# Optimization experiments

Measured on AMD Instinct MI355X. Metric: run time of the kernel, lower is better.

The kernel has to match this reference:

```python
import jax, jax.numpy as jnp
import numpy as np

N, F_IN, F_OUT = 8192, 256, 256
NEG_BIG = jnp.float32(-9e15)


def setup_inputs() -> dict:
    key = jax.random.key(0)
    k1, k2, k3, k4 = jax.random.split(key, 4)
    h = jax.random.normal(k1, (N, F_IN), dtype=jnp.float32)
    adj = jax.random.randint(k2, (N, N), 0, 2, dtype=jnp.int32)
    # nn.Linear(in, out): weight [out, in], bias [out]
    lim = 1.0 / np.sqrt(F_IN)
    W = jax.random.uniform(k3, (F_OUT, F_IN), dtype=jnp.float32, minval=-lim, maxval=lim)
    b = jax.random.uniform(k4, (F_OUT,), dtype=jnp.float32, minval=-lim, maxval=lim)
    return {"h": h, "adj": adj, "W": W, "b": b}


def reference(h, adj, W, b):
    n = h.shape[0]
    scale = 1.0 / jnp.sqrt(jnp.asarray(h.shape[1], h.dtype))
    # attention = h @ h.T / sqrt(d)   -> [N, N]
    att = jnp.matmul(h, h.T) * scale
    # masked softmax over rows
    A = jax.nn.softmax(jnp.where(adj > 0, att, NEG_BIG), axis=1)
    eye = jnp.eye(n, dtype=A.dtype)
    A = (A + eye) * 0.5
    # first `k` rows overwritten with identity, k = count of nonzeros in adj[:, 0]
    k = jnp.sum(adj[:, 0] != 0)
    row_is_identity = jnp.arange(n)[:, None] < k  # [N, 1] broadcast mask
    A = jnp.where(row_is_identity, eye, A)
    h_new = jnp.matmul(h, W.T) + b
    return jax.nn.relu(jnp.matmul(A, h_new))
```

## Files before the change

### kernel.cpp

```cpp
#include <hip/hip_runtime.h>


typedef __attribute__((ext_vector_type(8))) short short8;
typedef __attribute__((ext_vector_type(4))) float f32x4;

#define NN 8192
#define DD 256
#define NEGB -1.2983e16f

__device__ __forceinline__ unsigned short f2bf(float f) {
  unsigned u = __builtin_bit_cast(unsigned, f);
  u += 0x7FFFu + ((u >> 16) & 1u);
  return (unsigned short)(u >> 16);
}
__device__ __forceinline__ float bf2f(unsigned short s) {
  unsigned u = ((unsigned)s) << 16;
  return __builtin_bit_cast(float, u);
}
__device__ __forceinline__ f32x4 mfma16(short8 a, short8 b, f32x4 c) {
  return __builtin_amdgcn_mfma_f32_16x16x32_bf16(a, b, c, 0, 0, 0);
}
__device__ __forceinline__ void gld16(const unsigned short* g, unsigned short* l) {
  __builtin_amdgcn_global_load_lds(
      (const __attribute__((address_space(1))) void*)g,
      (__attribute__((address_space(3))) void*)l, 16, 0, 0);
}

__global__ __launch_bounds__(256) void count_k(const int* __restrict__ adj,
                                               int* __restrict__ kout) {
  __shared__ int red[256];
  int gid = blockIdx.x * 256 + threadIdx.x;
  red[threadIdx.x] = (adj[(size_t)gid * NN] != 0);
  __syncthreads();
  for (int off = 128; off; off >>= 1) {
    if (threadIdx.x < off) red[threadIdx.x] += red[threadIdx.x + off];
    __syncthreads();
  }
  if (threadIdx.x == 0) atomicAdd(kout, red[0]);
}

__global__ __launch_bounds__(256) void conv_h(const float* __restrict__ h,
                                              unsigned short* __restrict__ hQf) {
  int gid = blockIdx.x * 256 + threadIdx.x;
  int i = gid >> 6, k4 = (gid & 63) * 4;
  float4 v = *(const float4*)(h + (size_t)i * DD + k4);
  size_t off = ((size_t)((i >> 4) * 8 + (k4 >> 5)) * 64 +
                (((k4 >> 3) & 3) * 16 + (i & 15))) * 8 + (k4 & 7);
  ushort4 o;
  o.x = f2bf(v.x); o.y = f2bf(v.y); o.z = f2bf(v.z); o.w = f2bf(v.w);
  *(ushort4*)(hQf + off) = o;
}

__global__ __launch_bounds__(256) void pack_wf(const float* __restrict__ W,
                                               unsigned short* __restrict__ Wf) {
  int gid = blockIdx.x * 256 + threadIdx.x;
  int l = gid & 63, f = gid >> 6, n16 = f >> 3, kk = f & 7;
  int lr = l & 15, lg = l >> 4;
  const float* src = W + (size_t)(n16 * 16 + lr) * DD + kk * 32 + lg * 8;
  float4 w0 = *(const float4*)src, w1 = *(const float4*)(src + 4);
  short8 o;
  o[0] = (short)f2bf(w0.x); o[1] = (short)f2bf(w0.y);
  o[2] = (short)f2bf(w0.z); o[3] = (short)f2bf(w0.w);
  o[4] = (short)f2bf(w1.x); o[5] = (short)f2bf(w1.y);
  o[6] = (short)f2bf(w1.z); o[7] = (short)f2bf(w1.w);
  *(short8*)(Wf + (size_t)gid * 8) = o;
}

__global__ __launch_bounds__(256) void hnew_k(const unsigned short* __restrict__ hQf,
                                              const unsigned short* __restrict__ Wf,
                                              const float* __restrict__ bias,
                                              unsigned short* __restrict__ hnb,
                                              unsigned short* __restrict__ hnV) {
  const int tid = threadIdx.x, w = tid >> 6, l = tid & 63, lr = l & 15, lg = l >> 4;
  const int row0 = blockIdx.x * 64 + w * 16;

  short8 a[8];
#pragma unroll
  for (int kk = 0; kk < 8; ++kk)
    a[kk] = *(const short8*)(hQf + ((size_t)((row0 >> 4) * 8 + kk) * 64 + l) * 8);

  f32x4 acc[16];
#pragma unroll
  for (int nt = 0; nt < 16; ++nt) acc[nt] = (f32x4){0.f, 0.f, 0.f, 0.f};

#pragma unroll
  for (int kk = 0; kk < 8; ++kk)
#pragma unroll
    for (int nt = 0; nt < 16; ++nt) {
      short8 bf = *(const short8*)(Wf + ((size_t)(nt * 8 + kk) * 64 + l) * 8);
      acc[nt] = mfma16(a[kk], bf, acc[nt]);
    }
#pragma unroll
  for (int nt = 0; nt < 16; ++nt) {
    const int col = nt * 16 + lr;
    const float bv = bias[col];
#pragma unroll
    for (int q = 0; q < 4; ++q) {
      const int row = row0 + lg * 4 + q;
      unsigned short r16 = f2bf(acc[nt][q] + bv);
      hnb[(size_t)row * DD + col] = r16;
      hnV[((size_t)((row >> 5) * 16 + nt) * 64 + ((row >> 3) & 3) * 16 + lr) * 8 +
          (row & 7)] = r16;
    }
  }
}

__global__ __launch_bounds__(256, 2) void attn_k(
    const unsigned short* __restrict__ hQf, const unsigned short* __restrict__ hnV,
    const int* __restrict__ adj, const int* __restrict__ kptr,
    float* __restrict__ pl, unsigned short* __restrict__ pO, int T) {
  __shared__ __align__(16) unsigned short sK[2][8192];
  __shared__ __align__(16) unsigned short sV[2][8192];
  __shared__ __align__(16) unsigned short sP[4][16][40];

  const int tid = threadIdx.x, w = tid >> 6, l = tid & 63, lr = l & 15, lg = l >> 4;
  const int c = blockIdx.x, ty = blockIdx.y;
  const int i0 = ty * 64;
  const int kid = *kptr;
  if (i0 + 64 <= kid) return;

  const int r0 = i0 + w * 16;

  short8 qf[8];
#pragma unroll
  for (int kk = 0; kk < 8; ++kk)
    qf[kk] = *(const short8*)(hQf + ((size_t)((r0 >> 4) * 8 + kk) * 64 + l) * 8);

  f32x4 Oacc[16];
#pragma unroll
  for (int nt = 0; nt < 16; ++nt) Oacc[nt] = (f32x4){0.f, 0.f, 0.f, 0.f};
  float lsum[4] = {0.f, 0.f, 0.f, 0.f};
  const float c1 = 0.09016844005556021f;

  int arow[4];
#pragma unroll
  for (int q = 0; q < 4; ++q) arow[q] = (r0 + lg * 4 + q) * NN;

  const int jt0 = c * T;

  {
    const unsigned short* srcK = hQf + (size_t)jt0 * 8192;
    const unsigned short* srcV = hnV + (size_t)jt0 * 8192;
#pragma unroll
    for (int s = 0; s < 4; ++s) {
      const int so = (w * 4 + s) * 512;
      gld16(srcK + so + l * 8, &sK[0][so]);
      gld16(srcV + so + l * 8, &sV[0][so]);
    }
  }
  int avA[8], avB[8];
#pragma unroll
  for (int nt = 0; nt < 2; ++nt)
#pragma unroll
    for (int q = 0; q < 4; ++q)
      avA[nt * 4 + q] = adj[(size_t)arow[q] + jt0 * 32 + nt * 16 + lr];
  __syncthreads();

#define ATTN_ITER(T_IDX, CUR, MC, MN)                                          \
  {                                                                            \
    const int t_ = (T_IDX);                                                    \
    if (t_ + 1 < T) {    \
      const int jn = jt0 + t_ + 1;                                             \
      const unsigned short* srcK = hQf + (size_t)jn * 8192;                    \
      const unsigned short* srcV = hnV + (size_t)jn * 8192;                    \
      _Pragma("unroll") for (int s = 0; s < 4; ++s) {                          \
        const int so = (w * 4 + s) * 512;                                      \
        gld16(srcK + so + l * 8, &sK[(CUR) ^ 1][so]);                          \
        gld16(srcV + so + l * 8, &sV[(CUR) ^ 1][so]);                          \
      }                                                                        \
      _Pragma("unroll") for (int nt = 0; nt < 2; ++nt)                         \
        _Pragma("unroll") for (int q = 0; q < 4; ++q)                          \
          MN[nt * 4 + q] = adj[(size_t)arow[q] + jn * 32 + nt * 16 + lr];      \
    }                                                                          \
    f32x4 S2[2];                                                               \
    S2[0] = (f32x4){0.f, 0.f, 0.f, 0.f};                                       \
    S2[1] = (f32x4){0.f, 0.f, 0.f, 0.f};                                       \
    _Pragma("unroll") for (int kk = 0; kk < 8; ++kk)                           \
      _Pragma("unroll") for (int nt = 0; nt < 2; ++nt) {                       \
        short8 bf = *(const short8*)(&sK[(CUR)][(nt * 8 + kk) * 512 + l * 8]); \
        S2[nt] = mfma16(qf[kk], bf, S2[nt]);                                   \
      }                                                                        \
    float p0[4], p1[4];                                                        \
    _Pragma("unroll") for (int q = 0; q < 4; ++q) {                            \
      float sv0 = MC[q] ? fminf(S2[0][q] * c1, 60.f) : NEGB;                   \
      float sv1 = MC[4 + q] ? fminf(S2[1][q] * c1, 60.f) : NEGB;               \
      p0[q] = __builtin_amdgcn_exp2f(sv0);                                     \
      p1[q] = __builtin_amdgcn_exp2f(sv1);                                     \
      lsum[q] += p0[q] + p1[q];                                                \
    }                                                                          \
    _Pragma("unroll") for (int q = 0; q < 4; ++q) {                            \
      sP[w][lg * 4 + q][lr] = f2bf(p0[q]);                                     \
      sP[w][lg * 4 + q][16 + lr] = f2bf(p1[q]);                                \
    }                                                                          \
    short8 pa = *(const short8*)(&sP[w][lr][lg * 8]);                          \
    _Pragma("unroll") for (int cnt = 0; cnt < 16; ++cnt) {                     \
      short8 vf = *(const short8*)(&sV[(CUR)][cnt * 512 + l * 8]);             \
      Oacc[cnt] = mfma16(pa, vf, Oacc[cnt]);                                   \
    }                                                                          \
    __syncthreads();                                                           \
  }

  for (int tt = 0; tt < T; tt += 2) {
    ATTN_ITER(tt, 0, avA, avB);
    ATTN_ITER(tt + 1, 1, avB, avA);
  }
#undef ATTN_ITER

#pragma unroll
  for (int q = 0; q < 4; ++q) {
#pragma unroll
    for (int off = 1; off < 16; off <<= 1) lsum[q] += __shfl_xor(lsum[q], off);
    if (lr == 0) pl[(size_t)c * NN + r0 + lg * 4 + q] = lsum[q];
  }
#pragma unroll
  for (int cnt = 0; cnt < 16; ++cnt)
#pragma unroll
    for (int q = 0; q < 4; ++q) {
      int row = r0 + lg * 4 + q;
      pO[((size_t)c * NN + row) * DD + cnt * 16 + lr] = f2bf(Oacc[cnt][q]);
    }
}

__global__ __launch_bounds__(256) void comb_k(const float* __restrict__ pl,
                                              const unsigned short* __restrict__ pO,
                                              const unsigned short* __restrict__ hnb,
                                              const int* __restrict__ kptr,
                                              float* __restrict__ out, int S) {
  const int row = blockIdx.x * 4 + (threadIdx.x >> 6);
  const int col = (threadIdx.x & 63) * 4;
  const int kid = *kptr;
  ushort4 hv = *(const ushort4*)(hnb + (size_t)row * DD + col);
  float v0 = bf2f(hv.x), v1 = bf2f(hv.y), v2 = bf2f(hv.z), v3 = bf2f(hv.w);
  float4 r;
  if (row < kid) {
    r.x = v0; r.y = v1; r.z = v2; r.w = v3;
  } else {
    float L = 0.f, a0 = 0.f, a1 = 0.f, a2 = 0.f, a3 = 0.f;
    for (int cc = 0; cc < S; ++cc) {
      L += pl[(size_t)cc * NN + row];
      ushort4 ov = *(const ushort4*)(pO + ((size_t)cc * NN + row) * DD + col);
      a0 += bf2f(ov.x); a1 += bf2f(ov.y); a2 += bf2f(ov.z); a3 += bf2f(ov.w);
    }
    float inv = 0.5f / L;
    r.x = a0 * inv + 0.5f * v0; r.y = a1 * inv + 0.5f * v1;
    r.z = a2 * inv + 0.5f * v2; r.w = a3 * inv + 0.5f * v3;
  }
  r.x = fmaxf(r.x, 0.f); r.y = fmaxf(r.y, 0.f);
  r.z = fmaxf(r.z, 0.f); r.w = fmaxf(r.w, 0.f);
  *(float4*)(out + (size_t)row * DD + col) = r;
}

extern "C" void kernel_launch(void* const* d_in, const int* in_sizes, int n_in,
                              void* d_out, int out_size, void* d_ws, size_t ws_size,
                              hipStream_t stream) {
  const float* h = (const float*)d_in[0];
  const int* adj = (const int*)d_in[1];
  const float* W = (const float*)d_in[2];
  const float* b = (const float*)d_in[3];
  float* out = (float*)d_out;

  char* ws = (char*)d_ws;
  const size_t MB4 = (size_t)NN * DD * 2;
  int* kbuf = (int*)ws;
  unsigned short* hQf = (unsigned short*)(ws + 256);
  unsigned short* hnb = (unsigned short*)(ws + 256 + MB4);
  unsigned short* hnV = (unsigned short*)(ws + 256 + 2 * MB4);
  unsigned short* Wf = (unsigned short*)(ws + 256 + 3 * MB4);
  char* dyn = ws + 256 + 3 * MB4 + (256 << 10);

  size_t fixed = 256 + 3 * MB4 + (256 << 10);
  int S = 16;
  while (S > 1 && fixed + (size_t)S * NN * (DD * 2 + 4) > ws_size) S >>= 1;
  const int T = 256 / S;

  float* pl = (float*)dyn;
  unsigned short* pO = (unsigned short*)(pl + (size_t)S * NN);

  hipMemsetAsync(kbuf, 0, 4, stream);
  hipLaunchKernelGGL(count_k, dim3(32), dim3(256), 0, stream, adj, kbuf);
  hipLaunchKernelGGL(conv_h, dim3(2048), dim3(256), 0, stream, h, hQf);
  hipLaunchKernelGGL(pack_wf, dim3(32), dim3(256), 0, stream, W, Wf);
  hipLaunchKernelGGL(hnew_k, dim3(NN / 64), dim3(256), 0, stream, hQf, Wf, b, hnb, hnV);
  hipLaunchKernelGGL(attn_k, dim3(S, NN / 64), dim3(256), 0, stream,
                     hQf, hnV, adj, kbuf, pl, pO, T);
  hipLaunchKernelGGL(comb_k, dim3(NN / 4), dim3(256), 0, stream, pl, pO, hnb, kbuf, out, S);
}
```

Before: 117.5 us.

## Merge prep kernels, split hnew columns across blocks, raise MFMA wave priority

Three small preprocessing kernels (count, h conversion, W packing) become one launch that picks its role from the block index, removing two kernel launches. hnew_k now splits the 256 output columns across two blocks, doubling the grid to 256 blocks for better CU coverage, and writes hnV as ushort4 vectors instead of scalar stores. The attention loop wraps its MFMA sections in s_setprio so the waves issuing matrix ops get scheduling priority. The gains are small relative to the dominant attention kernel, and the priority hints may do nothing or cause interference.

```diff
diff --git a/kernel.cpp b/kernel.cpp
--- a/kernel.cpp
+++ b/kernel.cpp
@@ -26,44 +26,45 @@
       (__attribute__((address_space(3))) void*)l, 16, 0, 0);
 }
 
-__global__ __launch_bounds__(256) void count_k(const int* __restrict__ adj,
-                                               int* __restrict__ kout) {
-  __shared__ int red[256];
-  int gid = blockIdx.x * 256 + threadIdx.x;
-  red[threadIdx.x] = (adj[(size_t)gid * NN] != 0);
-  __syncthreads();
-  for (int off = 128; off; off >>= 1) {
-    if (threadIdx.x < off) red[threadIdx.x] += red[threadIdx.x + off];
+__global__ __launch_bounds__(256) void prep_k(const float* __restrict__ h,
+                                              const float* __restrict__ W,
+                                              const int* __restrict__ adj,
+                                              unsigned short* __restrict__ hQf,
+                                              unsigned short* __restrict__ Wf,
+                                              int* __restrict__ kout) {
+  const int bx = blockIdx.x, tid = threadIdx.x;
+  if (bx < 2048) {
+    int gid = bx * 256 + tid;
+    int i = gid >> 6, k4 = (gid & 63) * 4;
+    float4 v = *(const float4*)(h + (size_t)i * DD + k4);
+    size_t off = ((size_t)((i >> 4) * 8 + (k4 >> 5)) * 64 +
+                  (((k4 >> 3) & 3) * 16 + (i & 15))) * 8 + (k4 & 7);
+    ushort4 o;
+    o.x = f2bf(v.x); o.y = f2bf(v.y); o.z = f2bf(v.z); o.w = f2bf(v.w);
+    *(ushort4*)(hQf + off) = o;
+  } else if (bx < 2080) {
+    __shared__ int red[256];
+    int gid = (bx - 2048) * 256 + tid;
+    red[tid] = (adj[(size_t)gid * NN] != 0);
     __syncthreads();
-  }
-  if (threadIdx.x == 0) atomicAdd(kout, red[0]);
-}
-
-__global__ __launch_bounds__(256) void conv_h(const float* __restrict__ h,
-                                              unsigned short* __restrict__ hQf) {
-  int gid = blockIdx.x * 256 + threadIdx.x;
-  int i = gid >> 6, k4 = (gid & 63) * 4;
-  float4 v = *(const float4*)(h + (size_t)i * DD + k4);
-  size_t off = ((size_t)((i >> 4) * 8 + (k4 >> 5)) * 64 +
-                (((k4 >> 3) & 3) * 16 + (i & 15))) * 8 + (k4 & 7);
-  ushort4 o;
-  o.x = f2bf(v.x); o.y = f2bf(v.y); o.z = f2bf(v.z); o.w = f2bf(v.w);
-  *(ushort4*)(hQf + off) = o;
-}
-
-__global__ __launch_bounds__(256) void pack_wf(const float* __restrict__ W,
-                                               unsigned short* __restrict__ Wf) {
-  int gid = blockIdx.x * 256 + threadIdx.x;
-  int l = gid & 63, f = gid >> 6, n16 = f >> 3, kk = f & 7;
-  int lr = l & 15, lg = l >> 4;
-  const float* src = W + (size_t)(n16 * 16 + lr) * DD + kk * 32 + lg * 8;
-  float4 w0 = *(const float4*)src, w1 = *(const float4*)(src + 4);
-  short8 o;
-  o[0] = (short)f2bf(w0.x); o[1] = (short)f2bf(w0.y);
-  o[2] = (short)f2bf(w0.z); o[3] = (short)f2bf(w0.w);
-  o[4] = (short)f2bf(w1.x); o[5] = (short)f2bf(w1.y);
-  o[6] = (short)f2bf(w1.z); o[7] = (short)f2bf(w1.w);
-  *(short8*)(Wf + (size_t)gid * 8) = o;
+    for (int off = 128; off; off >>= 1) {
+      if (tid < off) red[tid] += red[tid + off];
+      __syncthreads();
+    }
+    if (tid == 0) atomicAdd(kout, red[0]);
+  } else {
+    int gid = (bx - 2080) * 256 + tid;
+    int l = gid & 63, f = gid >> 6, n16 = f >> 3, kk = f & 7;
+    int lr = l & 15, lg = l >> 4;
+    const float* src = W + (size_t)(n16 * 16 + lr) * DD + kk * 32 + lg * 8;
+    float4 w0 = *(const float4*)src, w1 = *(const float4*)(src + 4);
+    short8 o;
+    o[0] = (short)f2bf(w0.x); o[1] = (short)f2bf(w0.y);
+    o[2] = (short)f2bf(w0.z); o[3] = (short)f2bf(w0.w);
+    o[4] = (short)f2bf(w1.x); o[5] = (short)f2bf(w1.y);
+    o[6] = (short)f2bf(w1.z); o[7] = (short)f2bf(w1.w);
+    *(short8*)(Wf + (size_t)gid * 8) = o;
+  }
 }
 
 __global__ __launch_bounds__(256) void hnew_k(const unsigned short* __restrict__ hQf,
@@ -72,36 +73,38 @@
                                               unsigned short* __restrict__ hnb,
                                               unsigned short* __restrict__ hnV) {
   const int tid = threadIdx.x, w = tid >> 6, l = tid & 63, lr = l & 15, lg = l >> 4;
-  const int row0 = blockIdx.x * 64 + w * 16;
+  const int row0 = (blockIdx.x >> 1) * 64 + w * 16;
+  const int nt0 = (blockIdx.x & 1) * 8;
 
   short8 a[8];
 #pragma unroll
   for (int kk = 0; kk < 8; ++kk)
     a[kk] = *(const short8*)(hQf + ((size_t)((row0 >> 4) * 8 + kk) * 64 + l) * 8);
 
-  f32x4 acc[16];
-#pragma unroll
-  for (int nt = 0; nt < 16; ++nt) acc[nt] = (f32x4){0.f, 0.f, 0.f, 0.f};
+  f32x4 acc[8];
+#pragma unroll
+  for (int nt = 0; nt < 8; ++nt) acc[nt] = (f32x4){0.f, 0.f, 0.f, 0.f};
 
 #pragma unroll
   for (int kk = 0; kk < 8; ++kk)
 #pragma unroll
-    for (int nt = 0; nt < 16; ++nt) {
-      short8 bf = *(const short8*)(Wf + ((size_t)(nt * 8 + kk) * 64 + l) * 8);
+    for (int nt = 0; nt < 8; ++nt) {
+      short8 bf = *(const short8*)(Wf + ((size_t)((nt0 + nt) * 8 + kk) * 64 + l) * 8);
       acc[nt] = mfma16(a[kk], bf, acc[nt]);
     }
-#pragma unroll
-  for (int nt = 0; nt < 16; ++nt) {
-    const int col = nt * 16 + lr;
+  const int rowbase = row0 + lg * 4;
+#pragma unroll
+  for (int nt = 0; nt < 8; ++nt) {
+    const int col = (nt0 + nt) * 16 + lr;
     const float bv = bias[col];
-#pragma unroll
-    for (int q = 0; q < 4; ++q) {
-      const int row = row0 + lg * 4 + q;
-      unsigned short r16 = f2bf(acc[nt][q] + bv);
-      hnb[(size_t)row * DD + col] = r16;
-      hnV[((size_t)((row >> 5) * 16 + nt) * 64 + ((row >> 3) & 3) * 16 + lr) * 8 +
-          (row & 7)] = r16;
-    }
+    unsigned short r16[4];
+#pragma unroll
+    for (int q = 0; q < 4; ++q) r16[q] = f2bf(acc[nt][q] + bv);
+#pragma unroll
+    for (int q = 0; q < 4; ++q) hnb[(size_t)(rowbase + q) * DD + col] = r16[q];
+    ushort4 o4 = {r16[0], r16[1], r16[2], r16[3]};
+    *(ushort4*)(hnV + ((size_t)((rowbase >> 5) * 16 + nt0 + nt) * 64 +
+                       ((rowbase >> 3) & 3) * 16 + lr) * 8 + (rowbase & 7)) = o4;
   }
 }
 
@@ -175,11 +178,13 @@
     f32x4 S2[2];                                                               \
     S2[0] = (f32x4){0.f, 0.f, 0.f, 0.f};                                       \
     S2[1] = (f32x4){0.f, 0.f, 0.f, 0.f};                                       \
+    __builtin_amdgcn_s_setprio(1);                                             \
     _Pragma("unroll") for (int kk = 0; kk < 8; ++kk)                           \
       _Pragma("unroll") for (int nt = 0; nt < 2; ++nt) {                       \
         short8 bf = *(const short8*)(&sK[(CUR)][(nt * 8 + kk) * 512 + l * 8]); \
         S2[nt] = mfma16(qf[kk], bf, S2[nt]);                                   \
       }                                                                        \
+    __builtin_amdgcn_s_setprio(0);                                             \
     float p0[4], p1[4];                                                        \
     _Pragma("unroll") for (int q = 0; q < 4; ++q) {                            \
       float sv0 = MC[q] ? fminf(S2[0][q] * c1, 60.f) : NEGB;                   \
@@ -193,10 +198,12 @@
       sP[w][lg * 4 + q][16 + lr] = f2bf(p1[q]);                                \
     }                                                                          \
     short8 pa = *(const short8*)(&sP[w][lr][lg * 8]);                          \
+    __builtin_amdgcn_s_setprio(1);                                             \
     _Pragma("unroll") for (int cnt = 0; cnt < 16; ++cnt) {                     \
       short8 vf = *(const short8*)(&sV[(CUR)][cnt * 512 + l * 8]);             \
       Oacc[cnt] = mfma16(pa, vf, Oacc[cnt]);                                   \
     }                                                                          \
+    __builtin_amdgcn_s_setprio(0);                                             \
     __syncthreads();                                                           \
   }
 
@@ -277,10 +284,8 @@
   unsigned short* pO = (unsigned short*)(pl + (size_t)S * NN);
 
   hipMemsetAsync(kbuf, 0, 4, stream);
-  hipLaunchKernelGGL(count_k, dim3(32), dim3(256), 0, stream, adj, kbuf);
-  hipLaunchKernelGGL(conv_h, dim3(2048), dim3(256), 0, stream, h, hQf);
-  hipLaunchKernelGGL(pack_wf, dim3(32), dim3(256), 0, stream, W, Wf);
-  hipLaunchKernelGGL(hnew_k, dim3(NN / 64), dim3(256), 0, stream, hQf, Wf, b, hnb, hnV);
+  hipLaunchKernelGGL(prep_k, dim3(2112), dim3(256), 0, stream, h, W, adj, hQf, Wf, kbuf);
+  hipLaunchKernelGGL(hnew_k, dim3(256), dim3(256), 0, stream, hQf, Wf, b, hnb, hnV);
   hipLaunchKernelGGL(attn_k, dim3(S, NN / 64), dim3(256), 0, stream,
                      hQf, hnV, adj, kbuf, pl, pO, T);
   hipLaunchKernelGGL(comb_k, dim3(NN / 4), dim3(256), 0, stream, pl, pO, hnb, kbuf, out, S);
```

After: 106.1 us (median of 2 runs). 1.11x faster.
